# Kernel optimization log

Measured on AMD Instinct MI355X. Metric: run time of the kernel, lower is better.

## Reference

```python
import jax, jax.numpy as jnp
import numpy as np

TOKENS = 8192
MODEL_DIM = 4096
NUM_EXPERTS = 64
K = 2


def setup_inputs() -> dict:
    key = jax.random.key(0)
    kx, kw = jax.random.split(key)
    x = jax.random.normal(kx, (TOKENS, MODEL_DIM), dtype=jnp.float32)
    # nn.Linear default init: U(-1/sqrt(fan_in), 1/sqrt(fan_in)); weight shape [E, D]
    bound = 1.0 / np.sqrt(MODEL_DIM)
    W = jax.random.uniform(kw, (NUM_EXPERTS, MODEL_DIM), dtype=jnp.float32,
                           minval=-bound, maxval=bound)
    return {"x": x, "W": W}


def reference(x, W):
    # TopKGate.forward with k=2, eval mode (no noise): logits -> top2gating
    logits = jnp.einsum("td,ed->te", x.astype(jnp.float32), W)  # [T, E]
    # topk indices (sorted by value, like torch.topk)
    _, topi = jax.lax.top_k(logits, K)                           # [T, K]
    gates = jax.nn.softmax(logits, axis=-1)                      # [T, E]
    # (gates * one_hot(idx)).sum(-1) == gather of gates at idx
    g = jnp.take_along_axis(gates, topi, axis=-1)                # [T, K]
    eps = jnp.finfo(gates.dtype).eps
    denom = jnp.maximum(jnp.sum(g, axis=-1, keepdims=True), eps)
    g = g / denom
    # matches return ([idx1, idx2], [gate1, gate2]) with flattened indices
    return (topi[:, 0], topi[:, 1], g[:, 0], g[:, 1])
```

## Files before the change

kernel.cpp:

```cpp
#include <hip/hip_runtime.h>
#include <float.h>
#include <math.h>

#define TOKENS 8192
#define DIM    4096

typedef _Float16 v8h  __attribute__((ext_vector_type(8)));
typedef float    v4f  __attribute__((ext_vector_type(4)));

__global__ __launch_bounds__(256) void prep_w_kernel(
    const float* __restrict__ W, _Float16* __restrict__ WF) {
    int n = blockIdx.x * 256 + threadIdx.x;
    int chunk = n >> 8;
    int et    = (n >> 6) & 3;
    int lane  = n & 63;
    int e  = et * 16 + (lane & 15);
    int k0 = chunk * 32 + (lane >> 4) * 8;
    const float* src = W + (size_t)e * DIM + k0;
    v8h h, l;
    #pragma unroll
    for (int j = 0; j < 8; ++j) {
        float w = src[j];
        _Float16 wh = (_Float16)w;
        h[j] = wh;
        l[j] = (_Float16)((w - (float)wh) * 2048.0f);
    }
    size_t base = (size_t)chunk * 4096 + (size_t)et * 512 + (size_t)lane * 8;
    *(v8h*)(WF + base)        = h;
    *(v8h*)(WF + base + 2048) = l;
}

#define LOAD_A(Aa, Ab, cc) do {                                               \
    const float* ap_ = abase + (size_t)(cc) * 32;                             \
    Aa = *(const float4*)ap_;                                                 \
    Ab = *(const float4*)(ap_ + 4);                                           \
} while (0)

#define LOAD_B(BH, BL, cc) do {                                               \
    const _Float16* wp_ = wbase + (size_t)(cc) * 4096;                        \
    _Pragma("unroll")                                                         \
    for (int e_ = 0; e_ < 4; ++e_) {                                          \
        BH[e_] = *(const v8h*)(wp_ + e_ * 512);                               \
        BL[e_] = *(const v8h*)(wp_ + 2048 + e_ * 512);                        \
    }                                                                         \
} while (0)

#define COMP(Aa, Ab, BH, BL) do {                                             \
    float av_[8] = {Aa.x, Aa.y, Aa.z, Aa.w, Ab.x, Ab.y, Ab.z, Ab.w};          \
    v8h ah_, al_;                                                             \
    _Pragma("unroll")                                                         \
    for (int j_ = 0; j_ < 8; ++j_) {                                          \
        _Float16 h_ = (_Float16)av_[j_];                                      \
        ah_[j_] = h_;                                                         \
        al_[j_] = (_Float16)((av_[j_] - (float)h_) * 2048.0f);                \
    }                                                                         \
    _Pragma("unroll")                                                         \
    for (int e_ = 0; e_ < 4; ++e_)                                            \
        acc1[e_] = __builtin_amdgcn_mfma_f32_16x16x32_f16(ah_, BH[e_], acc1[e_], 0, 0, 0); \
    _Pragma("unroll")                                                         \
    for (int e_ = 0; e_ < 4; ++e_) {                                          \
        acc2[e_] = __builtin_amdgcn_mfma_f32_16x16x32_f16(al_, BH[e_], acc2[e_], 0, 0, 0); \
        acc2[e_] = __builtin_amdgcn_mfma_f32_16x16x32_f16(ah_, BL[e_], acc2[e_], 0, 0, 0); \
    }                                                                         \
} while (0)

__global__ __launch_bounds__(256, 2) void topkgate_kernel(
    const float* __restrict__ x,
    const _Float16* __restrict__ WF,
    float* __restrict__ out) {

    __shared__ float red[4][16][64];

    const int tid  = threadIdx.x;
    const int wq   = tid >> 6;
    const int lane = tid & 63;
    const int tok0 = blockIdx.x * 16;
    const int art  = lane & 15;
    const int akg  = lane >> 4;
    const int chunk0 = wq * 32;

    const float*    abase = x  + (size_t)(tok0 + art) * DIM + chunk0 * 32 + akg * 8;
    const _Float16* wbase = WF + (size_t)chunk0 * 4096 + (size_t)lane * 8;

    v4f acc1[4], acc2[4];
    #pragma unroll
    for (int e4 = 0; e4 < 4; ++e4) { acc1[e4] = (v4f)0.0f; acc2[e4] = (v4f)0.0f; }

    float4 A0a, A0b, A1a, A1b, A2a, A2b, A3a, A3b;
    v8h B0h[4], B0l[4], B1h[4], B1l[4];

    LOAD_A(A0a, A0b, 0);
    LOAD_A(A1a, A1b, 1);
    LOAD_A(A2a, A2b, 2);
    LOAD_A(A3a, A3b, 3);
    LOAD_B(B0h, B0l, 0);
    LOAD_B(B1h, B1l, 1);

    #pragma unroll 1
    for (int c = 0; c <= 24; c += 4) {
        COMP(A0a, A0b, B0h, B0l);  LOAD_A(A0a, A0b, c + 4);  LOAD_B(B0h, B0l, c + 2);
        COMP(A1a, A1b, B1h, B1l);  LOAD_A(A1a, A1b, c + 5);  LOAD_B(B1h, B1l, c + 3);
        COMP(A2a, A2b, B0h, B0l);  LOAD_A(A2a, A2b, c + 6);  LOAD_B(B0h, B0l, c + 4);
        COMP(A3a, A3b, B1h, B1l);  LOAD_A(A3a, A3b, c + 7);  LOAD_B(B1h, B1l, c + 5);
    }
    COMP(A0a, A0b, B0h, B0l);  LOAD_B(B0h, B0l, 30);
    COMP(A1a, A1b, B1h, B1l);  LOAD_B(B1h, B1l, 31);
    COMP(A2a, A2b, B0h, B0l);
    COMP(A3a, A3b, B1h, B1l);

    const float inv2048 = 1.0f / 2048.0f;
    #pragma unroll
    for (int e4 = 0; e4 < 4; ++e4) {
        #pragma unroll
        for (int r = 0; r < 4; ++r) {
            red[wq][akg * 4 + r][e4 * 16 + art] = acc1[e4][r] + acc2[e4][r] * inv2048;
        }
    }
    __syncthreads();

    #pragma unroll
    for (int tt = 0; tt < 4; ++tt) {
        int t = wq * 4 + tt;
        float v = red[0][t][lane] + red[1][t][lane]
                + red[2][t][lane] + red[3][t][lane];

        float bv = v; int bi = lane;
        #pragma unroll
        for (int off = 32; off >= 1; off >>= 1) {
            float ov = __shfl_xor(bv, off);
            int   oi = __shfl_xor(bi, off);
            if (ov > bv || (ov == bv && oi < bi)) { bv = ov; bi = oi; }
        }
        float v2 = (lane == bi) ? -FLT_MAX : v;
        float bv2 = v2; int bi2 = lane;
        #pragma unroll
        for (int off = 32; off >= 1; off >>= 1) {
            float ov = __shfl_xor(bv2, off);
            int   oi = __shfl_xor(bi2, off);
            if (ov > bv2 || (ov == bv2 && oi < bi2)) { bv2 = ov; bi2 = oi; }
        }

        if (lane == 0) {
            float g0 = 1.0f / (1.0f + expf(bv2 - bv));
            int gt = tok0 + t;
            out[gt]              = (float)bi;
            out[TOKENS + gt]     = (float)bi2;
            out[2 * TOKENS + gt] = g0;
            out[3 * TOKENS + gt] = 1.0f - g0;
        }
    }
}

extern "C" void kernel_launch(void* const* d_in, const int* in_sizes, int n_in,
                              void* d_out, int out_size, void* d_ws, size_t ws_size,
                              hipStream_t stream) {
    const float* x = (const float*)d_in[0];
    const float* W = (const float*)d_in[1];
    float* out     = (float*)d_out;
    _Float16* WF   = (_Float16*)d_ws;

    prep_w_kernel<<<128, 256, 0, stream>>>(W, WF);
    topkgate_kernel<<<TOKENS / 16, 256, 0, stream>>>(x, WF, out);
}
```

Baseline: 48.19 us.

## Split K across eight waves per block and restructure B prefetch pipeline

Doubles the block to 512 threads so each of eight waves reduces over 16 K-chunks instead of 32, and the cross-wave reduction now sums eight partials from a padded shared buffer. The B loads are split into half-tiles that are refetched right after use, which cuts the live B registers and lets occupancy rise to 4 blocks per CU. The loop is restructured with a sched_barrier before the A load. The cost is a larger shared-memory reduction and more partial accumulators to combine.

Measured after the change: 46.43 us. -3.7%, faster.

```diff
diff --git a/kernel.cpp b/kernel.cpp
--- a/kernel.cpp
+++ b/kernel.cpp
@@ -31,45 +31,69 @@
 }
 
 #define LOAD_A(Aa, Ab, cc) do {                                               \
-    const float* ap_ = abase + (size_t)(cc) * 32;                             \
+    const float* ap_ = abase + (cc) * 32;                                     \
     Aa = *(const float4*)ap_;                                                 \
     Ab = *(const float4*)(ap_ + 4);                                           \
 } while (0)
 
-#define LOAD_B(BH, BL, cc) do {                                               \
-    const _Float16* wp_ = wbase + (size_t)(cc) * 4096;                        \
-    _Pragma("unroll")                                                         \
-    for (int e_ = 0; e_ < 4; ++e_) {                                          \
-        BH[e_] = *(const v8h*)(wp_ + e_ * 512);                               \
-        BL[e_] = *(const v8h*)(wp_ + 2048 + e_ * 512);                        \
-    }                                                                         \
+#define LOAD_BH(H0, H1, L0, L1, cc, half) do {                                \
+    const _Float16* hp_ = wbH + (size_t)(cc) * 4096 + (half) * 1024;          \
+    const _Float16* lp_ = wbL + (size_t)(cc) * 4096 + (half) * 1024;          \
+    H0 = *(const v8h*)(hp_);                                                  \
+    H1 = *(const v8h*)(hp_ + 512);                                            \
+    L0 = *(const v8h*)(lp_);                                                  \
+    L1 = *(const v8h*)(lp_ + 512);                                            \
 } while (0)
 
-#define COMP(Aa, Ab, BH, BL) do {                                             \
-    float av_[8] = {Aa.x, Aa.y, Aa.z, Aa.w, Ab.x, Ab.y, Ab.z, Ab.w};          \
-    v8h ah_, al_;                                                             \
-    _Pragma("unroll")                                                         \
-    for (int j_ = 0; j_ < 8; ++j_) {                                          \
-        _Float16 h_ = (_Float16)av_[j_];                                      \
-        ah_[j_] = h_;                                                         \
-        al_[j_] = (_Float16)((av_[j_] - (float)h_) * 2048.0f);                \
-    }                                                                         \
-    _Pragma("unroll")                                                         \
-    for (int e_ = 0; e_ < 4; ++e_)                                            \
-        acc1[e_] = __builtin_amdgcn_mfma_f32_16x16x32_f16(ah_, BH[e_], acc1[e_], 0, 0, 0); \
-    _Pragma("unroll")                                                         \
-    for (int e_ = 0; e_ < 4; ++e_) {                                          \
-        acc2[e_] = __builtin_amdgcn_mfma_f32_16x16x32_f16(al_, BH[e_], acc2[e_], 0, 0, 0); \
-        acc2[e_] = __builtin_amdgcn_mfma_f32_16x16x32_f16(ah_, BL[e_], acc2[e_], 0, 0, 0); \
-    }                                                                         \
+#define CVT1(f, j) {                                                          \
+    _Float16 h_ = (_Float16)(f);                                              \
+    ah[j] = h_;                                                               \
+    al[j] = (_Float16)(((f) - (float)h_) * 2048.0f);                          \
+}
+#define CVT(Aa, Ab) do {                                                      \
+    CVT1(Aa.x, 0) CVT1(Aa.y, 1) CVT1(Aa.z, 2) CVT1(Aa.w, 3)                   \
+    CVT1(Ab.x, 4) CVT1(Ab.y, 5) CVT1(Ab.z, 6) CVT1(Ab.w, 7)                   \
 } while (0)
 
-__global__ __launch_bounds__(256, 2) void topkgate_kernel(
+#define COMP_HALF(e0, H0, H1, L0, L1) do {                                    \
+    acc1[e0]     = __builtin_amdgcn_mfma_f32_16x16x32_f16(ah, H0, acc1[e0], 0, 0, 0);     \
+    acc1[e0 + 1] = __builtin_amdgcn_mfma_f32_16x16x32_f16(ah, H1, acc1[e0 + 1], 0, 0, 0); \
+    acc2[e0]     = __builtin_amdgcn_mfma_f32_16x16x32_f16(al, H0, acc2[e0], 0, 0, 0);     \
+    acc2[e0]     = __builtin_amdgcn_mfma_f32_16x16x32_f16(ah, L0, acc2[e0], 0, 0, 0);     \
+    acc2[e0 + 1] = __builtin_amdgcn_mfma_f32_16x16x32_f16(al, H1, acc2[e0 + 1], 0, 0, 0); \
+    acc2[e0 + 1] = __builtin_amdgcn_mfma_f32_16x16x32_f16(ah, L1, acc2[e0 + 1], 0, 0, 0); \
+} while (0)
+
+#define CHUNK_FULL(AXa, AXb, cc) do {                                         \
+    CVT(AXa, AXb);                                                            \
+    COMP_HALF(0, B0a, B0b, B0c, B0d);                                         \
+    LOAD_BH(B0a, B0b, B0c, B0d, (cc) + 1, 0);                                 \
+    COMP_HALF(2, B1a, B1b, B1c, B1d);                                         \
+    LOAD_BH(B1a, B1b, B1c, B1d, (cc) + 1, 1);                                 \
+    __builtin_amdgcn_sched_barrier(0);                                        \
+    LOAD_A(AXa, AXb, (cc) + 4);                                               \
+} while (0)
+
+#define CHUNK_NB(AXa, AXb, cc) do {                  \
+    CVT(AXa, AXb);                                                            \
+    COMP_HALF(0, B0a, B0b, B0c, B0d);                                         \
+    LOAD_BH(B0a, B0b, B0c, B0d, (cc) + 1, 0);                                 \
+    COMP_HALF(2, B1a, B1b, B1c, B1d);                                         \
+    LOAD_BH(B1a, B1b, B1c, B1d, (cc) + 1, 1);                                 \
+} while (0)
+
+#define CHUNK_LAST(AXa, AXb) do {                         \
+    CVT(AXa, AXb);                                                            \
+    COMP_HALF(0, B0a, B0b, B0c, B0d);                                         \
+    COMP_HALF(2, B1a, B1b, B1c, B1d);                                         \
+} while (0)
+
+__global__ __launch_bounds__(512, 4) void topkgate_kernel(
     const float* __restrict__ x,
     const _Float16* __restrict__ WF,
     float* __restrict__ out) {
 
-    __shared__ float red[4][16][64];
+    __shared__ float red[8][16][65];
 
     const int tid  = threadIdx.x;
     const int wq   = tid >> 6;
@@ -77,36 +101,38 @@
     const int tok0 = blockIdx.x * 16;
     const int art  = lane & 15;
     const int akg  = lane >> 4;
-    const int chunk0 = wq * 32;
+    const int chunk0 = wq * 16;
 
-    const float*    abase = x  + (size_t)(tok0 + art) * DIM + chunk0 * 32 + akg * 8;
-    const _Float16* wbase = WF + (size_t)chunk0 * 4096 + (size_t)lane * 8;
+    const float*    abase = x   + (size_t)(tok0 + art) * DIM + chunk0 * 32 + akg * 8;
+    const _Float16* wbH   = WF  + (size_t)chunk0 * 4096 + (size_t)lane * 8;
+    const _Float16* wbL   = wbH + 2048;
 
     v4f acc1[4], acc2[4];
     #pragma unroll
     for (int e4 = 0; e4 < 4; ++e4) { acc1[e4] = (v4f)0.0f; acc2[e4] = (v4f)0.0f; }
 
     float4 A0a, A0b, A1a, A1b, A2a, A2b, A3a, A3b;
-    v8h B0h[4], B0l[4], B1h[4], B1l[4];
+    v8h B0a, B0b, B0c, B0d, B1a, B1b, B1c, B1d;
+    v8h ah, al;
 
+    LOAD_BH(B0a, B0b, B0c, B0d, 0, 0);
+    LOAD_BH(B1a, B1b, B1c, B1d, 0, 1);
     LOAD_A(A0a, A0b, 0);
     LOAD_A(A1a, A1b, 1);
     LOAD_A(A2a, A2b, 2);
     LOAD_A(A3a, A3b, 3);
-    LOAD_B(B0h, B0l, 0);
-    LOAD_B(B1h, B1l, 1);
 
     #pragma unroll 1
-    for (int c = 0; c <= 24; c += 4) {
-        COMP(A0a, A0b, B0h, B0l);  LOAD_A(A0a, A0b, c + 4);  LOAD_B(B0h, B0l, c + 2);
-        COMP(A1a, A1b, B1h, B1l);  LOAD_A(A1a, A1b, c + 5);  LOAD_B(B1h, B1l, c + 3);
-        COMP(A2a, A2b, B0h, B0l);  LOAD_A(A2a, A2b, c + 6);  LOAD_B(B0h, B0l, c + 4);
-        COMP(A3a, A3b, B1h, B1l);  LOAD_A(A3a, A3b, c + 7);  LOAD_B(B1h, B1l, c + 5);
+    for (int c = 0; c < 12; c += 4) {
+        CHUNK_FULL(A0a, A0b, c);
+        CHUNK_FULL(A1a, A1b, c + 1);
+        CHUNK_FULL(A2a, A2b, c + 2);
+        CHUNK_FULL(A3a, A3b, c + 3);
     }
-    COMP(A0a, A0b, B0h, B0l);  LOAD_B(B0h, B0l, 30);
-    COMP(A1a, A1b, B1h, B1l);  LOAD_B(B1h, B1l, 31);
-    COMP(A2a, A2b, B0h, B0l);
-    COMP(A3a, A3b, B1h, B1l);
+    CHUNK_NB(A0a, A0b, 12);
+    CHUNK_NB(A1a, A1b, 13);
+    CHUNK_NB(A2a, A2b, 14);
+    CHUNK_LAST(A3a, A3b);
 
     const float inv2048 = 1.0f / 2048.0f;
     #pragma unroll
@@ -119,10 +145,12 @@
     __syncthreads();
 
     #pragma unroll
-    for (int tt = 0; tt < 4; ++tt) {
-        int t = wq * 4 + tt;
+    for (int tt = 0; tt < 2; ++tt) {
+        int t = wq * 2 + tt;
         float v = red[0][t][lane] + red[1][t][lane]
-                + red[2][t][lane] + red[3][t][lane];
+                + red[2][t][lane] + red[3][t][lane]
+                + red[4][t][lane] + red[5][t][lane]
+                + red[6][t][lane] + red[7][t][lane];
 
         float bv = v; int bi = lane;
         #pragma unroll
@@ -160,5 +188,5 @@
     _Float16* WF   = (_Float16*)d_ws;
 
     prep_w_kernel<<<128, 256, 0, stream>>>(W, WF);
-    topkgate_kernel<<<TOKENS / 16, 256, 0, stream>>>(x, WF, out);
+    topkgate_kernel<<<TOKENS / 16, 512, 0, stream>>>(x, WF, out);
 }
```
